# Optimization experiments

Measured on AMD Instinct MI355X. Metric: run time of the kernel, lower is better.

Reference implementation:

```python
import jax, jax.numpy as jnp
import numpy as np

C = 256
CK = C // 8  # key/query channels


def setup_inputs() -> dict:
    key = jax.random.key(0)
    ks = jax.random.split(key, 7)
    B, H, W = 8, 64, 64
    x = jax.random.normal(ks[0], (B, C, H, W), dtype=jnp.float32)
    # 1x1 conv weights (out_ch, in_ch) and biases. Spectral norm is a weight
    # reparameterization; at forward time it is just a conv with (normalized)
    # weights, so we sample weights directly.
    Wf = jax.random.normal(ks[1], (CK, C), dtype=jnp.float32) * 0.02
    bf = jnp.zeros((CK,), dtype=jnp.float32)
    Wg = jax.random.normal(ks[2], (CK, C), dtype=jnp.float32) * 0.02
    bg = jnp.zeros((CK,), dtype=jnp.float32)
    Wh = jax.random.normal(ks[3], (C, C), dtype=jnp.float32) * 0.02
    bh = jnp.zeros((C,), dtype=jnp.float32)
    gamma = jnp.ones((1,), dtype=jnp.float32) * 0.5  # nonzero so attention path matters
    return {"x": x, "Wf": Wf, "bf": bf, "Wg": Wg, "bg": bg, "Wh": Wh, "bh": bh, "gamma": gamma}


def reference(x, Wf, bf, Wg, bg, Wh, bh, gamma):
    b, c, h, w = x.shape
    n = h * w
    xf = x.reshape(b, c, n)  # [B, C, N]
    # 1x1 convs == per-pixel linear maps
    fx = jnp.einsum("kc,bcn->bkn", Wf, xf) + bf[None, :, None]  # [B, CK, N]
    gx = jnp.einsum("kc,bcn->bkn", Wg, xf) + bg[None, :, None]  # [B, CK, N]
    hx = jnp.einsum("oc,bcn->bon", Wh, xf) + bh[None, :, None]  # [B, C, N]
    # sx[b, i, j] = <fx[:, i], gx[:, j]>
    sx = jnp.einsum("bki,bkj->bij", fx, gx)  # [B, N, N]
    # torch F.softmax(sx, dim=1): normalize over the first N axis (i)
    beta = jax.nn.softmax(sx, axis=1)
    ox = jnp.einsum("bci,bij->bcj", hx, beta).reshape(b, c, h, w)
    return gamma.reshape(()) * ox + x
```

## Files before the change

kernel.cpp:

```cpp
#include <hip/hip_runtime.h>
#include <stdint.h>


typedef __bf16 bf16;
typedef __bf16 bf16x2 __attribute__((ext_vector_type(2)));
typedef __bf16 bf16x8 __attribute__((ext_vector_type(8)));
typedef float  f32x16 __attribute__((ext_vector_type(16)));
typedef float  f32x4  __attribute__((ext_vector_type(4)));

#define BATCH 8
#define CC    256
#define CKK   32
#define NN    4096
#define LOG2E 1.4426950408889634f

__device__ __forceinline__ f32x16 zero16() {
  f32x16 z;
#pragma unroll
  for (int i = 0; i < 16; ++i) z[i] = 0.0f;
  return z;
}

__device__ __forceinline__ unsigned pack2(float lo, float hi) {
  bf16x2 v = {(bf16)lo, (bf16)hi};
  return __builtin_bit_cast(unsigned, v);
}

__device__ __forceinline__ f32x16 mfma32(bf16x8 a, bf16x8 b, f32x16 c) {
  return __builtin_amdgcn_mfma_f32_32x32x16_bf16(a, b, c, 0, 0, 0);
}

#define GLDS16(srcp, dstp)                                                         \
  __builtin_amdgcn_global_load_lds(                                               \
      (const __attribute__((address_space(1))) void*)(srcp),                      \
      (__attribute__((address_space(3))) void*)(dstp), 16, 0, 0)

__global__ __launch_bounds__(256) void k_transpose(const float* __restrict__ x,
                                                   bf16* __restrict__ xT) {
  __shared__ float tile[64][65];
  const int n0 = blockIdx.x * 64;
  const int c0 = blockIdx.y * 64;
  const int b  = blockIdx.z;
  const int t = threadIdx.x;
  const int tn = t & 63, trow = t >> 6;
#pragma unroll
  for (int i = 0; i < 16; ++i) {
    int c = trow + i * 4;
    tile[c][tn] = x[((size_t)(b * CC + c0 + c)) * NN + n0 + tn];
  }
  __syncthreads();
#pragma unroll
  for (int i = 0; i < 16; ++i) {
    int n = trow + i * 4;
    xT[((size_t)(b * NN + n0 + n)) * CC + c0 + tn] = (bf16)tile[tn][n];
  }
}

__global__ __launch_bounds__(64) void k_wprep(const float* __restrict__ Wf, const float* __restrict__ bfv,
                                              const float* __restrict__ Wg, const float* __restrict__ bg,
                                              const float* __restrict__ Wh, const float* __restrict__ bh,
                                              bf16* __restrict__ Wcat, float* __restrict__ bcat) {
  const int ko = blockIdx.x;
  const int t = threadIdx.x;
  const float* src;
  float scale = 1.0f;
  if (ko < 32) src = Wf + (size_t)ko * CC;
  else if (ko < 64) { src = Wg + (size_t)(ko - 32) * CC; scale = LOG2E; }
  else src = Wh + (size_t)(ko - 64) * CC;
#pragma unroll
  for (int i = 0; i < 4; ++i)
    Wcat[(size_t)ko * CC + t + i * 64] = (bf16)(src[t + i * 64] * scale);
  if (ko == 0) {
    for (int i = t; i < 320; i += 64) {
      float v = (i < 32) ? bfv[i] : (i < 64) ? bg[i - 32] * LOG2E : bh[i - 64];
      bcat[i] = v;
    }
  }
}

__global__ __launch_bounds__(256, 1) void k_proj(const bf16* __restrict__ xT,
                                                 const bf16* __restrict__ Wcat,
                                                 const float* __restrict__ bcat,
                                                 bf16* __restrict__ fxT, bf16* __restrict__ gxT,
                                                 bf16* __restrict__ hx) {
  const int d = blockIdx.x;
  const int b = d & 7, nb = d >> 3;
  const int t = threadIdx.x;
  const int w = t >> 6, ln = t & 63, ln31 = ln & 31, h = ln >> 5;
  const int n = nb * 128 + w * 32 + ln31;

  f32x16 acc[10];
#pragma unroll
  for (int mt = 0; mt < 10; ++mt) acc[mt] = zero16();

  const bf16* xrow = xT + ((size_t)(b * NN + n)) * CC;
#pragma unroll
  for (int ks = 0; ks < 16; ++ks) {
    bf16x8 bfrag = *(const bf16x8*)(xrow + ks * 16 + h * 8);
#pragma unroll
    for (int mt = 0; mt < 10; ++mt) {
      bf16x8 afrag = *(const bf16x8*)(Wcat + (size_t)(mt * 32 + ln31) * CC + ks * 16 + h * 8);
      acc[mt] = mfma32(afrag, bfrag, acc[mt]);
    }
  }

#pragma unroll
  for (int mt = 0; mt < 10; ++mt) {
#pragma unroll
    for (int q = 0; q < 4; ++q) {
      const int ko0 = mt * 32 + 8 * q + 4 * h;
      float v0 = acc[mt][4 * q + 0] + bcat[ko0 + 0];
      float v1 = acc[mt][4 * q + 1] + bcat[ko0 + 1];
      float v2 = acc[mt][4 * q + 2] + bcat[ko0 + 2];
      float v3 = acc[mt][4 * q + 3] + bcat[ko0 + 3];
      if (mt < 2) {
        bf16* dst = (mt == 0 ? fxT : gxT) + ((size_t)(b * NN + n)) * CKK + (8 * q + 4 * h);
        uint2 pv;
        pv.x = pack2(v0, v1);
        pv.y = pack2(v2, v3);
        *(uint2*)dst = pv;
      } else {
        const int c = ko0 - 64;
        hx[((size_t)(b * CC + c + 0)) * NN + n] = (bf16)v0;
        hx[((size_t)(b * CC + c + 1)) * NN + n] = (bf16)v1;
        hx[((size_t)(b * CC + c + 2)) * NN + n] = (bf16)v2;
        hx[((size_t)(b * CC + c + 3)) * NN + n] = (bf16)v3;
      }
    }
  }
}

__global__ __launch_bounds__(512, 2) void k_attn(const bf16* __restrict__ fxT,
                                                 const bf16* __restrict__ gxT,
                                                 const bf16* __restrict__ hx,
                                                 const float* __restrict__ x,
                                                 const float* __restrict__ gammap,
                                                 float* __restrict__ out) {
  extern __shared__ __align__(16) char smem[];
  __shared__ float lsh[128];
  const int d = blockIdx.x;
  const int b = d & 7, jb = d >> 3;
  const int t = threadIdx.x;
  const int g = t >> 8;
  const int tg = t & 255;
  const int wg = tg >> 6;
  const int ln = t & 63, ln31 = ln & 31, h = ln >> 5;
  const int j = jb * 128 + wg * 32 + ln31;
  const int kbase = g * 2048;

  const bf16* fxb = fxT + (size_t)b * NN * CKK;
  const bf16* hxb = hx + (size_t)b * CC * NN;

  bf16* vsg = (bf16*)smem + g * 32768;
  bf16* ksg = (bf16*)(smem + 131072) + g * 4096;

  const bf16* qrow = gxT + ((size_t)b * NN + j) * CKK;
  bf16x8 qf0 = *(const bf16x8*)(qrow + h * 8);
  bf16x8 qf1 = *(const bf16x8*)(qrow + 16 + h * 8);
  asm volatile("" ::: "memory");

  const int tau = (ln31 >> 1) & 3;
  const int vo0 = ln31 * 32 + ((h ^ tau) * 8);
  const int vo1 = ln31 * 32 + (((2 + h) ^ tau) * 8);

  const int lrow = ln >> 2;
  const int lcol = ((ln & 3) ^ ((ln >> 3) & 3)) * 8;
  const bf16* vlane = hxb + (size_t)(wg * 64 + lrow) * NN + lcol;
  const bf16* klane = fxb + (size_t)(wg * 16 + lrow) * CKK + lcol;

#define STAGEV(sidx, i0s)                                                     \
  {                                                                            \
    _Pragma("unroll")                                                          \
    for (int q = 0; q < 4; ++q)                                                \
      GLDS16(vlane + (size_t)q * 16 * NN + (i0s),                              \
             vsg + (sidx) * 8192 + (wg * 64 + q * 16) * 32);                   \
  }
#define STAGEK(sidx, i0s)                                                     \
  {                                                                            \
    if (wg < 2)                                                                \
      GLDS16(klane + (size_t)(i0s) * CKK, ksg + (sidx) * 1024 + wg * 512);     \
  }

  f32x16 oacc[8];
#pragma unroll
  for (int ct = 0; ct < 8; ++ct) oacc[ct] = zero16();
  float l_run = 0.0f;

  auto QK = [&](int slot) -> f32x16 {
    const bf16* kt = ksg + slot * 1024;
    bf16x8 kf0 = *(const bf16x8*)(kt + vo0);
    bf16x8 kf1 = *(const bf16x8*)(kt + vo1);
    f32x16 s = zero16();
    s = mfma32(kf0, qf0, s);
    s = mfma32(kf1, qf1, s);
    return s;
  };
  auto SM = [&](const f32x16& s, bf16x8* pf) {
    float ls0 = 0.0f, ls1 = 0.0f;
    unsigned pk[4][2];
#pragma unroll
    for (int q = 0; q < 4; ++q)
#pragma unroll
      for (int wi = 0; wi < 2; ++wi) {
        float a0 = __builtin_exp2f(s[4 * q + 2 * wi]);
        float a1 = __builtin_exp2f(s[4 * q + 2 * wi + 1]);
        ls0 += a0; ls1 += a1;
        pk[q][wi] = pack2(a0, a1);
      }
    float lsum = ls0 + ls1;
    lsum += __shfl_xor(lsum, 32);
    l_run += lsum;
#pragma unroll
    for (int ks = 0; ks < 2; ++ks) {
      union { unsigned u[4]; bf16x8 v; } pu;
#pragma unroll
      for (int wi = 0; wi < 2; ++wi) {
        unsigned xx = pk[2 * ks][wi];
        unsigned yy = pk[2 * ks + 1][wi];
        asm("v_permlane32_swap_b32 %0, %1" : "+v"(xx), "+v"(yy));
        pu.u[wi]     = xx;
        pu.u[2 + wi] = yy;
      }
      pf[ks] = pu.v;
    }
  };
  auto PV = [&](const bf16x8* pf, int slot) {
    const bf16* vb = vsg + slot * 8192;
    __builtin_amdgcn_s_setprio(1);
#pragma unroll
    for (int ct = 0; ct < 8; ++ct) {
      const bf16* vrow = vb + ct * 1024;
      oacc[ct] = mfma32(*(const bf16x8*)(vrow + vo0), pf[0], oacc[ct]);
      oacc[ct] = mfma32(*(const bf16x8*)(vrow + vo1), pf[1], oacc[ct]);
    }
    __builtin_amdgcn_s_setprio(0);
  };

  STAGEV(0, kbase); STAGEK(0, kbase);
  STAGEV(1, kbase + 32); STAGEK(1, kbase + 32);
  STAGEK(2, kbase + 64);
  asm volatile("s_waitcnt vmcnt(0)" ::: "memory");
  __builtin_amdgcn_s_barrier();
  asm volatile("" ::: "memory");

  f32x16 s_cur = QK(0);
  bf16x8 pfs[2];
  bf16x8 pft[2];

  for (int kb = 0; kb < 64; ++kb) {
    if (wg < 2) { asm volatile("s_waitcnt vmcnt(5)" ::: "memory"); }
    else        { asm volatile("s_waitcnt vmcnt(4)" ::: "memory"); }
    __builtin_amdgcn_s_barrier();
    asm volatile("" ::: "memory");

    STAGEV((kb + 2) & 3, kbase + ((kb + 2) & 63) * 32);
    STAGEK((kb + 3) & 3, kbase + ((kb + 3) & 63) * 32);

    if (g == 0) {
      SM(s_cur, pft);
      PV(pft, kb & 3);
    } else {
      if (kb > 0) PV(pfs, (kb - 1) & 3);
      SM(s_cur, pfs);
    }
    s_cur = QK((kb + 1) & 3);
  }
  if (g == 1) PV(pfs, 63 & 3);

  asm volatile("s_waitcnt vmcnt(0) lgkmcnt(0)" ::: "memory");
  __builtin_amdgcn_s_barrier();
  asm volatile("" ::: "memory");

  float* obuf = (float*)smem;
  const int jl = wg * 32 + ln31;
  if (g == 1) {
#pragma unroll
    for (int ct = 0; ct < 8; ++ct)
#pragma unroll
      for (int q = 0; q < 4; ++q) {
        f32x4 v;
        v[0] = oacc[ct][4 * q + 0];
        v[1] = oacc[ct][4 * q + 1];
        v[2] = oacc[ct][4 * q + 2];
        v[3] = oacc[ct][4 * q + 3];
        *(f32x4*)&obuf[jl * 260 + ct * 32 + 8 * q + 4 * h] = v;
      }
    if (h == 0) lsh[jl] = l_run;
  }
  __syncthreads();
  if (g == 0) {
    const float l = l_run + lsh[jl];
    const float ginv = gammap[0] / l;
    const float* xb = x + (size_t)b * CC * NN;
    float* ob = out + (size_t)b * CC * NN;
#pragma unroll
    for (int ct = 0; ct < 8; ++ct)
#pragma unroll
      for (int q = 0; q < 4; ++q) {
        f32x4 vB = *(const f32x4*)&obuf[jl * 260 + ct * 32 + 8 * q + 4 * h];
#pragma unroll
        for (int s = 0; s < 4; ++s) {
          int c = ct * 32 + 8 * q + 4 * h + s;
          size_t idx = (size_t)c * NN + j;
          float val = oacc[ct][4 * q + s] + vB[s];
          ob[idx] = fmaf(ginv, val, xb[idx]);
        }
      }
  }
#undef STAGEV
#undef STAGEK
}

extern "C" void kernel_launch(void* const* d_in, const int* in_sizes, int n_in,
                              void* d_out, int out_size, void* d_ws, size_t ws_size,
                              hipStream_t stream) {
  const float* x     = (const float*)d_in[0];
  const float* Wf    = (const float*)d_in[1];
  const float* bfv   = (const float*)d_in[2];
  const float* Wg    = (const float*)d_in[3];
  const float* bg    = (const float*)d_in[4];
  const float* Wh    = (const float*)d_in[5];
  const float* bh    = (const float*)d_in[6];
  const float* gamma = (const float*)d_in[7];
  float* out = (float*)d_out;

  char* ws = (char*)d_ws;
  bf16* fxT  = (bf16*)(ws);
  bf16* gxT  = (bf16*)(ws + 2097152);
  bf16* hx   = (bf16*)(ws + 4194304);
  bf16* Wcat = (bf16*)(ws + 20971520);
  float* bcat = (float*)(ws + 21135360);
  bf16* xT = (bf16*)d_out;

  k_transpose<<<dim3(64, 4, 8), 256, 0, stream>>>(x, xT);
  k_wprep<<<dim3(320), 64, 0, stream>>>(Wf, bfv, Wg, bg, Wh, bh, Wcat, bcat);
  k_proj<<<dim3(256), 256, 0, stream>>>(xT, Wcat, bcat, fxT, gxT, hx);
  k_attn<<<dim3(256), 512, 147456, stream>>>(fxT, gxT, hx, x, gamma, out);
}
```

Baseline: 150.8 us.

## Process 64-key blocks with two-phase ping-pong schedule between wave groups

```diff
diff --git a/kernel.cpp b/kernel.cpp
--- a/kernel.cpp
+++ b/kernel.cpp
@@ -152,120 +152,147 @@
   const bf16* hxb = hx + (size_t)b * CC * NN;
 
   bf16* vsg = (bf16*)smem + g * 32768;
-  bf16* ksg = (bf16*)(smem + 131072) + g * 4096;
+  bf16* ksg = (bf16*)(smem + 131072) + g * 6144;
 
   const bf16* qrow = gxT + ((size_t)b * NN + j) * CKK;
   bf16x8 qf0 = *(const bf16x8*)(qrow + h * 8);
   bf16x8 qf1 = *(const bf16x8*)(qrow + 16 + h * 8);
   asm volatile("" ::: "memory");
 
-  const int tau = (ln31 >> 1) & 3;
-  const int vo0 = ln31 * 32 + ((h ^ tau) * 8);
-  const int vo1 = ln31 * 32 + (((2 + h) ^ tau) * 8);
-
-  const int lrow = ln >> 2;
-  const int lcol = ((ln & 3) ^ ((ln >> 3) & 3)) * 8;
-  const bf16* vlane = hxb + (size_t)(wg * 64 + lrow) * NN + lcol;
-  const bf16* klane = fxb + (size_t)(wg * 16 + lrow) * CKK + lcol;
-
-#define STAGEV(sidx, i0s)                                                     \
+  int voff[4];
+#pragma unroll
+  for (int ks = 0; ks < 4; ++ks)
+    voff[ks] = ln31 * 64 + (((2 * ks + h) ^ (ln31 & 7)) * 8);
+  const int tk = (ln31 >> 1) & 3;
+  const int ko0 = ln31 * 32 + ((h ^ tk) * 8);
+  const int ko1 = ln31 * 32 + (((2 + h) ^ tk) * 8);
+
+  const int vrow_l = ln >> 3;
+  const int vcol_l = ((ln & 7) ^ ((ln >> 3) & 7)) * 8;
+  const bf16* vlane = hxb + (size_t)(wg * 64 + vrow_l) * NN + vcol_l;
+  const int krow_l = ln >> 2;
+  const int kcol_l = ((ln & 3) ^ ((ln >> 3) & 3)) * 8;
+  const bf16* klane = fxb + (size_t)(wg * 16 + krow_l) * CKK + kcol_l;
+
+#define STAGEV(slot, i0s)                                                     \
   {                                                                            \
     _Pragma("unroll")                                                          \
-    for (int q = 0; q < 4; ++q)                                                \
-      GLDS16(vlane + (size_t)q * 16 * NN + (i0s),                              \
-             vsg + (sidx) * 8192 + (wg * 64 + q * 16) * 32);                   \
-  }
-#define STAGEK(sidx, i0s)                                                     \
-  {                                                                            \
-    if (wg < 2)                                                                \
-      GLDS16(klane + (size_t)(i0s) * CKK, ksg + (sidx) * 1024 + wg * 512);     \
-  }
+    for (int q = 0; q < 8; ++q)                                                \
+      GLDS16(vlane + (size_t)q * 8 * NN + (i0s),                               \
+             vsg + (slot) * 16384 + (wg * 64 + q * 8) * 64);                   \
+  }
+#define STAGEK(kslot, i0s)                                                    \
+  { GLDS16(klane + (size_t)(i0s) * CKK, ksg + (kslot) * 2048 + wg * 16 * 32); }
 
   f32x16 oacc[8];
 #pragma unroll
   for (int ct = 0; ct < 8; ++ct) oacc[ct] = zero16();
   float l_run = 0.0f;
-
-  auto QK = [&](int slot) -> f32x16 {
-    const bf16* kt = ksg + slot * 1024;
-    bf16x8 kf0 = *(const bf16x8*)(kt + vo0);
-    bf16x8 kf1 = *(const bf16x8*)(kt + vo1);
-    f32x16 s = zero16();
-    s = mfma32(kf0, qf0, s);
-    s = mfma32(kf1, qf1, s);
-    return s;
+  bf16x8 pf[4] = {};
+
+  auto QK = [&](int kslot, f32x16& s0, f32x16& s1) {
+    const bf16* kt = ksg + kslot * 2048;
+    bf16x8 kf00 = *(const bf16x8*)(kt + ko0);
+    bf16x8 kf01 = *(const bf16x8*)(kt + ko1);
+    bf16x8 kf10 = *(const bf16x8*)(kt + 1024 + ko0);
+    bf16x8 kf11 = *(const bf16x8*)(kt + 1024 + ko1);
+    s0 = zero16(); s1 = zero16();
+    s0 = mfma32(kf00, qf0, s0);
+    s0 = mfma32(kf01, qf1, s0);
+    s1 = mfma32(kf10, qf0, s1);
+    s1 = mfma32(kf11, qf1, s1);
   };
-  auto SM = [&](const f32x16& s, bf16x8* pf) {
-    float ls0 = 0.0f, ls1 = 0.0f;
-    unsigned pk[4][2];
+  auto SM = [&](const f32x16& s0, const f32x16& s1) {
+    float ls0 = 0.0f, ls1 = 0.0f, ls2 = 0.0f, ls3 = 0.0f;
+    unsigned pk0[4][2], pk1[4][2];
 #pragma unroll
     for (int q = 0; q < 4; ++q)
 #pragma unroll
       for (int wi = 0; wi < 2; ++wi) {
-        float a0 = __builtin_exp2f(s[4 * q + 2 * wi]);
-        float a1 = __builtin_exp2f(s[4 * q + 2 * wi + 1]);
-        ls0 += a0; ls1 += a1;
-        pk[q][wi] = pack2(a0, a1);
-      }
-    float lsum = ls0 + ls1;
-    lsum += __shfl_xor(lsum, 32);
-    l_run += lsum;
+        float a0 = __builtin_exp2f(s0[4 * q + 2 * wi]);
+        float a1 = __builtin_exp2f(s0[4 * q + 2 * wi + 1]);
+        float b0 = __builtin_exp2f(s1[4 * q + 2 * wi]);
+        float b1 = __builtin_exp2f(s1[4 * q + 2 * wi + 1]);
+        ls0 += a0; ls1 += a1; ls2 += b0; ls3 += b1;
+        pk0[q][wi] = pack2(a0, a1);
+        pk1[q][wi] = pack2(b0, b1);
+      }
+    l_run += (ls0 + ls1) + (ls2 + ls3);
 #pragma unroll
     for (int ks = 0; ks < 2; ++ks) {
-      union { unsigned u[4]; bf16x8 v; } pu;
+      union { unsigned u[4]; bf16x8 v; } pa, pb;
 #pragma unroll
       for (int wi = 0; wi < 2; ++wi) {
-        unsigned xx = pk[2 * ks][wi];
-        unsigned yy = pk[2 * ks + 1][wi];
-        asm("v_permlane32_swap_b32 %0, %1" : "+v"(xx), "+v"(yy));
-        pu.u[wi]     = xx;
-        pu.u[2 + wi] = yy;
-      }
-      pf[ks] = pu.v;
+        unsigned x0 = pk0[2 * ks][wi],     y0 = pk0[2 * ks + 1][wi];
+        asm("v_permlane32_swap_b32 %0, %1" : "+v"(x0), "+v"(y0));
+        pa.u[wi] = x0; pa.u[2 + wi] = y0;
+        unsigned x1 = pk1[2 * ks][wi],     y1 = pk1[2 * ks + 1][wi];
+        asm("v_permlane32_swap_b32 %0, %1" : "+v"(x1), "+v"(y1));
+        pb.u[wi] = x1; pb.u[2 + wi] = y1;
+      }
+      pf[ks] = pa.v;
+      pf[2 + ks] = pb.v;
     }
   };
-  auto PV = [&](const bf16x8* pf, int slot) {
-    const bf16* vb = vsg + slot * 8192;
+  auto PV = [&](int slot) {
+    const bf16* vb = vsg + slot * 16384;
+    bf16x8 va0, va1, va2, va3, vn0, vn1, vn2, vn3;
+    va0 = *(const bf16x8*)(vb + voff[0]);
+    va1 = *(const bf16x8*)(vb + voff[1]);
+    va2 = *(const bf16x8*)(vb + voff[2]);
+    va3 = *(const bf16x8*)(vb + voff[3]);
     __builtin_amdgcn_s_setprio(1);
 #pragma unroll
     for (int ct = 0; ct < 8; ++ct) {
-      const bf16* vrow = vb + ct * 1024;
-      oacc[ct] = mfma32(*(const bf16x8*)(vrow + vo0), pf[0], oacc[ct]);
-      oacc[ct] = mfma32(*(const bf16x8*)(vrow + vo1), pf[1], oacc[ct]);
+      if (ct < 7) {
+        const bf16* vrow = vb + (ct + 1) * 2048;
+        vn0 = *(const bf16x8*)(vrow + voff[0]);
+        vn1 = *(const bf16x8*)(vrow + voff[1]);
+        vn2 = *(const bf16x8*)(vrow + voff[2]);
+        vn3 = *(const bf16x8*)(vrow + voff[3]);
+      }
+      oacc[ct] = mfma32(va0, pf[0], oacc[ct]);
+      oacc[ct] = mfma32(va1, pf[1], oacc[ct]);
+      oacc[ct] = mfma32(va2, pf[2], oacc[ct]);
+      oacc[ct] = mfma32(va3, pf[3], oacc[ct]);
+      va0 = vn0; va1 = vn1; va2 = vn2; va3 = vn3;
     }
     __builtin_amdgcn_s_setprio(0);
   };
 
-  STAGEV(0, kbase); STAGEK(0, kbase);
-  STAGEV(1, kbase + 32); STAGEK(1, kbase + 32);
-  STAGEK(2, kbase + 64);
-  asm volatile("s_waitcnt vmcnt(0)" ::: "memory");
-  __builtin_amdgcn_s_barrier();
-  asm volatile("" ::: "memory");
-
-  f32x16 s_cur = QK(0);
-  bf16x8 pfs[2];
-  bf16x8 pft[2];
-
-  for (int kb = 0; kb < 64; ++kb) {
-    if (wg < 2) { asm volatile("s_waitcnt vmcnt(5)" ::: "memory"); }
-    else        { asm volatile("s_waitcnt vmcnt(4)" ::: "memory"); }
+  STAGEV(0, kbase);
+  STAGEK(0, kbase);
+  STAGEK(1, kbase + 64);
+
+  for (int kb = 0; kb < 32; ++kb) {
+    asm volatile("s_waitcnt vmcnt(0)" ::: "memory");
     __builtin_amdgcn_s_barrier();
     asm volatile("" ::: "memory");
 
-    STAGEV((kb + 2) & 3, kbase + ((kb + 2) & 63) * 32);
-    STAGEK((kb + 3) & 3, kbase + ((kb + 3) & 63) * 32);
-
+    f32x16 s0, s1;
     if (g == 0) {
-      SM(s_cur, pft);
-      PV(pft, kb & 3);
+      QK(kb % 3, s0, s1);
+      SM(s0, s1);
+    } else if (kb > 0) {
+      PV((kb - 1) & 1);
+    }
+
+    __builtin_amdgcn_s_barrier();
+    asm volatile("" ::: "memory");
+
+    STAGEV((kb + 1) & 1, kbase + ((kb + 1) & 31) * 64);
+    STAGEK((kb + 2) % 3, kbase + ((kb + 2) & 31) * 64);
+
+    if (g == 0) {
+      PV(kb & 1);
     } else {
-      if (kb > 0) PV(pfs, (kb - 1) & 3);
-      SM(s_cur, pfs);
-    }
-    s_cur = QK((kb + 1) & 3);
-  }
-  if (g == 1) PV(pfs, 63 & 3);
+      QK(kb % 3, s0, s1);
+      SM(s0, s1);
+    }
+  }
+  if (g == 1) PV(31 & 1);
+
+  l_run += __shfl_xor(l_run, 32);
 
   asm volatile("s_waitcnt vmcnt(0) lgkmcnt(0)" ::: "memory");
   __builtin_amdgcn_s_barrier();
@@ -335,5 +362,5 @@
   k_transpose<<<dim3(64, 4, 8), 256, 0, stream>>>(x, xT);
   k_wprep<<<dim3(320), 64, 0, stream>>>(Wf, bfv, Wg, bg, Wh, bh, Wcat, bcat);
   k_proj<<<dim3(256), 256, 0, stream>>>(xT, Wcat, bcat, fxT, gxT, hx);
-  k_attn<<<dim3(256), 512, 147456, stream>>>(fxT, gxT, hx, x, gamma, out);
-}
+  k_attn<<<dim3(256), 512, 155648, stream>>>(fxT, gxT, hx, x, gamma, out);
+}
```

Result: faster. 145.6 us (-3.4%).
